# Kernel tuning notes

Hardware: AMD Instinct MI355X
Metric: run time of the kernel (lower is better)

The kernel has to match this reference:

```python
import jax, jax.numpy as jnp
import numpy as np

TEMPERATURE = 0.5
NEG_FILL = -9e15


def setup_inputs() -> dict:
    key = jax.random.key(0)
    k1, k2 = jax.random.split(key)
    B, D = 8192, 128
    z_i = jax.random.normal(k1, (B, D), dtype=jnp.float32)
    z_j = jax.random.normal(k2, (B, D), dtype=jnp.float32)
    return {"z_i": z_i, "z_j": z_j}


def reference(z_i, z_j):
    B = z_i.shape[0]
    N = 2 * B
    z = jnp.concatenate([z_i, z_j], axis=0)              # [2B, D]
    sim = jnp.matmul(z, z.T) / TEMPERATURE               # [2B, 2B]
    # mask out self-similarity on the diagonal
    diag = jnp.eye(N, dtype=bool)
    sim = jnp.where(diag, NEG_FILL, sim)
    # positive pair of row k is row (k+B) mod 2B
    labels = jnp.concatenate([jnp.arange(B, N), jnp.arange(0, B)])
    # CrossEntropyLoss(reduction='sum'): sum_k logsumexp(sim[k]) - sim[k, labels[k]]
    lse = jax.nn.logsumexp(sim, axis=1)                  # [2B]
    pos = sim[jnp.arange(N), labels]                     # [2B]
    loss = jnp.sum(lse - pos)
    return loss / N
```

## Files before the change

kernel.cpp:

```cpp
#include <hip/hip_runtime.h>

#define TEMP    0.5f
#define LOG2E   1.4426950408889634f
#define C2      (LOG2E / TEMP)
#define SQC2    1.6986436f
#define MSHIFT  160.0f
#define LN2     0.6931471805599453f
#define NROWS   16384
#define BHALF   8192
#define DDIM    128
#define PREPB   2048
#define MAINB   512

typedef __bf16 bf16x8 __attribute__((ext_vector_type(8)));
typedef float  f32x16 __attribute__((ext_vector_type(16)));
typedef float  f32x2  __attribute__((ext_vector_type(2)));

__device__ __forceinline__ float fexp2(float x) {
#if __has_builtin(__builtin_amdgcn_exp2f)
  return __builtin_amdgcn_exp2f(x);
#else
  return exp2f(x);
#endif
}

__device__ __forceinline__ unsigned short f2bf(float f) {
  unsigned int u = __float_as_uint(f);
  unsigned int r = (u + 0x7FFFu + ((u >> 16) & 1u)) >> 16;
  return (unsigned short)r;
}


__global__ void k_prep(const float* __restrict__ zi, const float* __restrict__ zj,
                       unsigned short* __restrict__ zbF,
                       float* __restrict__ S, float* __restrict__ Pp,
                       unsigned int* __restrict__ cnt) {
  const int t   = blockIdx.x * 256 + threadIdx.x;
  const int row = t >> 5;
  const int k0  = (t & 31) * 4;
  const float* src = (row < BHALF) ? (zi + (size_t)row * DDIM)
                                   : (zj + (size_t)(row - BHALF) * DDIM);
  float4 v = *reinterpret_cast<const float4*>(src + k0);

  const int g = row >> 5, lo = row & 31, khi = k0 >> 3, j0 = k0 & 7;
  ushort4 o;
  o.x = f2bf(v.x * SQC2); o.y = f2bf(v.y * SQC2);
  o.z = f2bf(v.z * SQC2); o.w = f2bf(v.w * SQC2);
  *reinterpret_cast<ushort4*>(zbF + (size_t)g * 4096 + khi * 256 + lo * 8 + j0) = o;

  float dot = 0.f;
  if (row < BHALF) {
    float4 w = *reinterpret_cast<const float4*>(zj + (size_t)row * DDIM + k0);
    dot = fmaf(v.x, w.x, fmaf(v.y, w.y, fmaf(v.z, w.z, v.w * w.w)));
  }
#pragma unroll
  for (int m = 32; m >= 1; m >>= 1) dot += __shfl_xor(dot, m, 64);
  __shared__ float red[4];
  if ((threadIdx.x & 63) == 0) red[threadIdx.x >> 6] = dot;
  __syncthreads();
  if (threadIdx.x == 0) Pp[blockIdx.x] = red[0] + red[1] + red[2] + red[3];

  if (t < NROWS) S[t] = 0.f;
  if (t == 0) cnt[0] = 0u;
}

template <bool MASK>
__device__ __forceinline__ void expAcc(const f32x16& acc, f32x2& s, int d, int hi) {
#pragma unroll
  for (int k = 0; k < 8; ++k) {
    f32x2 e;
    e.x = fexp2(acc[2 * k]);
    e.y = fexp2(acc[2 * k + 1]);
    if (MASK) {
      const int r0 = 2 * k, r1 = 2 * k + 1;
      if (((r0 & 3) + 8 * (r0 >> 2) + 4 * hi) == d) e.x = 0.f;
      if (((r1 & 3) + 8 * (r1 >> 2) + 4 * hi) == d) e.y = 0.f;
    }
    s += e;
  }
}

#define MFMA_ __builtin_amdgcn_mfma_f32_32x32x16_bf16

__global__ __launch_bounds__(256, 2)
void k_main(const unsigned short* __restrict__ zbF, float* __restrict__ S,
            const float* __restrict__ Pp, unsigned int* __restrict__ cnt,
            float* __restrict__ out) {
  const int wave = threadIdx.x >> 6;
  const int lane = threadIdx.x & 63;
  const int lo = lane & 31;
  const int hi = lane >> 5;
  const int rb = blockIdx.x & 31;
  const int cc = blockIdx.x >> 5;
  const int row0w = rb * 512 + wave * 128;

  bf16x8 b[4][8];
#pragma unroll
  for (int rt = 0; rt < 4; ++rt) {
    const unsigned short* bp = zbF + (size_t)((row0w >> 5) + rt) * 4096 + hi * 256 + lo * 8;
#pragma unroll
    for (int ks = 0; ks < 8; ++ks)
      b[rt][ks] = *reinterpret_cast<const bf16x8*>(bp + ks * 512);
  }

  f32x16 kC;
#pragma unroll
  for (int r = 0; r < 16; ++r) kC[r] = -MSHIFT;

  f32x2 s[4];
#pragma unroll
  for (int rt = 0; rt < 4; ++rt) { s[rt].x = 0.f; s[rt].y = 0.f; }

  const int c0base = cc * 1024;
  const unsigned short* abase = zbF + (size_t)(c0base >> 5) * 4096 + hi * 256 + lo * 8;

  bf16x8 a[8];
#pragma unroll
  for (int ks = 0; ks < 8; ++ks)
    a[ks] = *reinterpret_cast<const bf16x8*>(abase + ks * 512);

  if (((blockIdx.x ^ wave) & 1) != 0) __builtin_amdgcn_s_sleep(4);

  for (int it = 0; it < 32; ++it) {
    const int c0 = c0base + it * 32;
    const int dr = c0 - row0w;
    const bool dg = (unsigned)dr < 128u;
    const int rtd = dg ? (dr >> 5) : -1;

    __builtin_amdgcn_s_setprio(1);
    f32x16 acc0 = MFMA_(a[0], b[0][0], kC, 0, 0, 0);
    f32x16 acc1 = MFMA_(a[0], b[1][0], kC, 0, 0, 0);
#pragma unroll
    for (int ks = 1; ks < 8; ++ks) {
      acc0 = MFMA_(a[ks], b[0][ks], acc0, 0, 0, 0);
      acc1 = MFMA_(a[ks], b[1][ks], acc1, 0, 0, 0);
    }
    __builtin_amdgcn_s_setprio(0);
    if (!dg) {
      expAcc<false>(acc0, s[0], -1, hi);
      expAcc<false>(acc1, s[1], -1, hi);
    } else {
      expAcc<true>(acc0, s[0], rtd == 0 ? lo : -1, hi);
      expAcc<true>(acc1, s[1], rtd == 1 ? lo : -1, hi);
    }

    __builtin_amdgcn_s_setprio(1);
    acc0 = MFMA_(a[0], b[2][0], kC, 0, 0, 0);
    acc1 = MFMA_(a[0], b[3][0], kC, 0, 0, 0);
#pragma unroll
    for (int ks = 1; ks < 8; ++ks) {
      acc0 = MFMA_(a[ks], b[2][ks], acc0, 0, 0, 0);
      acc1 = MFMA_(a[ks], b[3][ks], acc1, 0, 0, 0);
    }
    __builtin_amdgcn_s_setprio(0);

    if (it + 1 < 32) {
      const unsigned short* ap = abase + (size_t)(it + 1) * 4096;
#pragma unroll
      for (int ks = 0; ks < 8; ++ks)
        a[ks] = *reinterpret_cast<const bf16x8*>(ap + ks * 512);
    }

    if (!dg) {
      expAcc<false>(acc0, s[2], -1, hi);
      expAcc<false>(acc1, s[3], -1, hi);
    } else {
      expAcc<true>(acc0, s[2], rtd == 2 ? lo : -1, hi);
      expAcc<true>(acc1, s[3], rtd == 3 ? lo : -1, hi);
    }
  }

#pragma unroll
  for (int rt = 0; rt < 4; ++rt) {
    float v = s[rt].x + s[rt].y;
    v += __shfl_xor(v, 32, 64);
    if (hi == 0) atomicAdd(&S[row0w + rt * 32 + lo], v);
  }

  asm volatile("s_waitcnt vmcnt(0)" ::: "memory");
  __syncthreads();
  __shared__ unsigned int lastFlag;
  if (threadIdx.x == 0) {
    unsigned int old = __hip_atomic_fetch_add(cnt, 1u, __ATOMIC_RELAXED,
                                              __HIP_MEMORY_SCOPE_AGENT);
    lastFlag = (old == (unsigned)(MAINB - 1)) ? 1u : 0u;
  }
  __syncthreads();
  if (lastFlag) {
    __threadfence();
    const int t = threadIdx.x;
    float q = 0.f;
    for (int r = t; r < NROWS; r += 256) {
      float sv = __hip_atomic_load(&S[r], __ATOMIC_RELAXED,
                                   __HIP_MEMORY_SCOPE_AGENT);
      q += LN2 * (MSHIFT + __log2f(sv));
    }
    for (int r = t; r < PREPB; r += 256)
      q -= 4.0f * Pp[r];
    __shared__ float red[256];
    red[t] = q;
    __syncthreads();
    for (int s2 = 128; s2 > 0; s2 >>= 1) {
      if (t < s2) red[t] += red[t + s2];
      __syncthreads();
    }
    if (t == 0) out[0] = red[0] / (float)NROWS;
  }
}

extern "C" void kernel_launch(void* const* d_in, const int* in_sizes, int n_in,
                              void* d_out, int out_size, void* d_ws, size_t ws_size,
                              hipStream_t stream) {
  const float* zi = (const float*)d_in[0];
  const float* zj = (const float*)d_in[1];
  unsigned short* zbF = (unsigned short*)d_ws;
  float* S  = (float*)((char*)d_ws + (size_t)NROWS * DDIM * 2);
  float* Pp = S + NROWS;
  unsigned int* cnt = (unsigned int*)(Pp + PREPB);
  float* out = (float*)d_out;

  hipLaunchKernelGGL(k_prep, dim3(PREPB), dim3(256), 0, stream, zi, zj, zbF, S, Pp, cnt);
  hipLaunchKernelGGL(k_main, dim3(MAINB), dim3(256), 0, stream, zbF, S, Pp, cnt, out);
}
```

Baseline: 144.0 us.

## Fuse prep and main kernels into one persistent kernel with grid barrier

Measured after the change: 210.0 us. 45.8% more time.

```diff
diff --git a/kernel.cpp b/kernel.cpp
--- a/kernel.cpp
+++ b/kernel.cpp
@@ -3,13 +3,12 @@
 #define TEMP    0.5f
 #define LOG2E   1.4426950408889634f
 #define C2      (LOG2E / TEMP)
-#define SQC2    1.6986436f
 #define MSHIFT  160.0f
 #define LN2     0.6931471805599453f
 #define NROWS   16384
 #define BHALF   8192
 #define DDIM    128
-#define PREPB   2048
+#define NCHUNK  2048
 #define MAINB   512
 
 typedef __bf16 bf16x8 __attribute__((ext_vector_type(8)));
@@ -31,46 +30,19 @@
 }
 
 
-__global__ void k_prep(const float* __restrict__ zi, const float* __restrict__ zj,
-                       unsigned short* __restrict__ zbF,
-                       float* __restrict__ S, float* __restrict__ Pp,
-                       unsigned int* __restrict__ cnt) {
-  const int t   = blockIdx.x * 256 + threadIdx.x;
-  const int row = t >> 5;
-  const int k0  = (t & 31) * 4;
-  const float* src = (row < BHALF) ? (zi + (size_t)row * DDIM)
-                                   : (zj + (size_t)(row - BHALF) * DDIM);
-  float4 v = *reinterpret_cast<const float4*>(src + k0);
-
-  const int g = row >> 5, lo = row & 31, khi = k0 >> 3, j0 = k0 & 7;
-  ushort4 o;
-  o.x = f2bf(v.x * SQC2); o.y = f2bf(v.y * SQC2);
-  o.z = f2bf(v.z * SQC2); o.w = f2bf(v.w * SQC2);
-  *reinterpret_cast<ushort4*>(zbF + (size_t)g * 4096 + khi * 256 + lo * 8 + j0) = o;
-
-  float dot = 0.f;
-  if (row < BHALF) {
-    float4 w = *reinterpret_cast<const float4*>(zj + (size_t)row * DDIM + k0);
-    dot = fmaf(v.x, w.x, fmaf(v.y, w.y, fmaf(v.z, w.z, v.w * w.w)));
-  }
-#pragma unroll
-  for (int m = 32; m >= 1; m >>= 1) dot += __shfl_xor(dot, m, 64);
-  __shared__ float red[4];
-  if ((threadIdx.x & 63) == 0) red[threadIdx.x >> 6] = dot;
-  __syncthreads();
-  if (threadIdx.x == 0) Pp[blockIdx.x] = red[0] + red[1] + red[2] + red[3];
-
-  if (t < NROWS) S[t] = 0.f;
-  if (t == 0) cnt[0] = 0u;
-}
-
 template <bool MASK>
 __device__ __forceinline__ void expAcc(const f32x16& acc, f32x2& s, int d, int hi) {
 #pragma unroll
   for (int k = 0; k < 8; ++k) {
+    f32x2 u;
+    u.x = acc[2 * k];
+    u.y = acc[2 * k + 1];
+    const f32x2 c2v = {C2, C2};
+    const f32x2 msv = {-MSHIFT, -MSHIFT};
+    u = __builtin_elementwise_fma(u, c2v, msv);
     f32x2 e;
-    e.x = fexp2(acc[2 * k]);
-    e.y = fexp2(acc[2 * k + 1]);
+    e.x = fexp2(u.x);
+    e.y = fexp2(u.y);
     if (MASK) {
       const int r0 = 2 * k, r1 = 2 * k + 1;
       if (((r0 & 3) + 8 * (r0 >> 2) + 4 * hi) == d) e.x = 0.f;
@@ -83,9 +55,63 @@
 #define MFMA_ __builtin_amdgcn_mfma_f32_32x32x16_bf16
 
 __global__ __launch_bounds__(256, 2)
-void k_main(const unsigned short* __restrict__ zbF, float* __restrict__ S,
-            const float* __restrict__ Pp, unsigned int* __restrict__ cnt,
-            float* __restrict__ out) {
+void k_all(const float* __restrict__ zi, const float* __restrict__ zj,
+           unsigned short* __restrict__ zbF, float* __restrict__ S,
+           float* __restrict__ Pp, unsigned int* __restrict__ cnt,
+           float* __restrict__ out) {
+  __shared__ unsigned int curChunk;
+  __shared__ float red[4];
+
+  unsigned int nmine = 0;
+  for (;;) {
+    if (threadIdx.x == 0)
+      curChunk = __hip_atomic_fetch_add(&cnt[0], 1u, __ATOMIC_RELAXED,
+                                        __HIP_MEMORY_SCOPE_AGENT);
+    __syncthreads();
+    const unsigned int c = curChunk;
+    if (c >= NCHUNK) break;
+
+    const int t   = (int)c * 256 + threadIdx.x;
+    const int row = t >> 5;
+    const int k0  = (t & 31) * 4;
+    const float* src = (row < BHALF) ? (zi + (size_t)row * DDIM)
+                                     : (zj + (size_t)(row - BHALF) * DDIM);
+    float4 v = *reinterpret_cast<const float4*>(src + k0);
+
+    const int g = row >> 5, lo2 = row & 31, khi = k0 >> 3, j0 = k0 & 7;
+    ushort4 o;
+    o.x = f2bf(v.x); o.y = f2bf(v.y); o.z = f2bf(v.z); o.w = f2bf(v.w);
+    *reinterpret_cast<ushort4*>(zbF + (size_t)g * 4096 + khi * 256 + lo2 * 8 + j0) = o;
+
+    float dot = 0.f;
+    if (row < BHALF) {
+      float4 w = *reinterpret_cast<const float4*>(zj + (size_t)row * DDIM + k0);
+      dot = fmaf(v.x, w.x, fmaf(v.y, w.y, fmaf(v.z, w.z, v.w * w.w)));
+    }
+#pragma unroll
+    for (int m = 32; m >= 1; m >>= 1) dot += __shfl_xor(dot, m, 64);
+    if ((threadIdx.x & 63) == 0) red[threadIdx.x >> 6] = dot;
+    __syncthreads();
+    if (threadIdx.x == 0) Pp[c] = red[0] + red[1] + red[2] + red[3];
+    if (t < NROWS) S[t] = 0.f;
+    ++nmine;
+    __syncthreads();
+  }
+
+  __builtin_amdgcn_fence(__ATOMIC_RELEASE, "agent");
+  __syncthreads();
+  if (threadIdx.x == 0 && nmine)
+    __hip_atomic_fetch_add(&cnt[1], nmine, __ATOMIC_RELAXED,
+                           __HIP_MEMORY_SCOPE_AGENT);
+
+  if (threadIdx.x == 0) {
+    while (__hip_atomic_load(&cnt[1], __ATOMIC_RELAXED,
+                             __HIP_MEMORY_SCOPE_AGENT) < NCHUNK)
+      __builtin_amdgcn_s_sleep(16);
+  }
+  __syncthreads();
+  __builtin_amdgcn_fence(__ATOMIC_ACQUIRE, "agent");
+
   const int wave = threadIdx.x >> 6;
   const int lane = threadIdx.x & 63;
   const int lo = lane & 31;
@@ -103,10 +129,7 @@
       b[rt][ks] = *reinterpret_cast<const bf16x8*>(bp + ks * 512);
   }
 
-  f32x16 kC;
-#pragma unroll
-  for (int r = 0; r < 16; ++r) kC[r] = -MSHIFT;
-
+  const f32x16 kZ = {};
   f32x2 s[4];
 #pragma unroll
   for (int rt = 0; rt < 4; ++rt) { s[rt].x = 0.f; s[rt].y = 0.f; }
@@ -128,8 +151,8 @@
     const int rtd = dg ? (dr >> 5) : -1;
 
     __builtin_amdgcn_s_setprio(1);
-    f32x16 acc0 = MFMA_(a[0], b[0][0], kC, 0, 0, 0);
-    f32x16 acc1 = MFMA_(a[0], b[1][0], kC, 0, 0, 0);
+    f32x16 acc0 = MFMA_(a[0], b[0][0], kZ, 0, 0, 0);
+    f32x16 acc1 = MFMA_(a[0], b[1][0], kZ, 0, 0, 0);
 #pragma unroll
     for (int ks = 1; ks < 8; ++ks) {
       acc0 = MFMA_(a[ks], b[0][ks], acc0, 0, 0, 0);
@@ -145,8 +168,8 @@
     }
 
     __builtin_amdgcn_s_setprio(1);
-    acc0 = MFMA_(a[0], b[2][0], kC, 0, 0, 0);
-    acc1 = MFMA_(a[0], b[3][0], kC, 0, 0, 0);
+    acc0 = MFMA_(a[0], b[2][0], kZ, 0, 0, 0);
+    acc1 = MFMA_(a[0], b[3][0], kZ, 0, 0, 0);
 #pragma unroll
     for (int ks = 1; ks < 8; ++ks) {
       acc0 = MFMA_(a[ks], b[2][ks], acc0, 0, 0, 0);
@@ -181,30 +204,34 @@
   __syncthreads();
   __shared__ unsigned int lastFlag;
   if (threadIdx.x == 0) {
-    unsigned int old = __hip_atomic_fetch_add(cnt, 1u, __ATOMIC_RELAXED,
+    unsigned int old = __hip_atomic_fetch_add(&cnt[2], 1u, __ATOMIC_RELAXED,
                                               __HIP_MEMORY_SCOPE_AGENT);
     lastFlag = (old == (unsigned)(MAINB - 1)) ? 1u : 0u;
   }
   __syncthreads();
   if (lastFlag) {
-    __threadfence();
+    __builtin_amdgcn_fence(__ATOMIC_ACQUIRE, "agent");
     const int t = threadIdx.x;
     float q = 0.f;
-    for (int r = t; r < NROWS; r += 256) {
-      float sv = __hip_atomic_load(&S[r], __ATOMIC_RELAXED,
-                                   __HIP_MEMORY_SCOPE_AGENT);
-      q += LN2 * (MSHIFT + __log2f(sv));
-    }
-    for (int r = t; r < PREPB; r += 256)
-      q -= 4.0f * Pp[r];
-    __shared__ float red[256];
-    red[t] = q;
+    const float4* S4 = reinterpret_cast<const float4*>(S);
+    for (int i = t; i < NROWS / 4; i += 256) {
+      float4 sv = S4[i];
+      q += LN2 * (4.0f * MSHIFT + __log2f(sv.x) + __log2f(sv.y) +
+                  __log2f(sv.z) + __log2f(sv.w));
+    }
+    const float4* P4 = reinterpret_cast<const float4*>(Pp);
+    for (int i = t; i < NCHUNK / 4; i += 256) {
+      float4 p = P4[i];
+      q -= 4.0f * (p.x + p.y + p.z + p.w);
+    }
+    __shared__ float redf[256];
+    redf[t] = q;
     __syncthreads();
     for (int s2 = 128; s2 > 0; s2 >>= 1) {
-      if (t < s2) red[t] += red[t + s2];
+      if (t < s2) redf[t] += redf[t + s2];
       __syncthreads();
     }
-    if (t == 0) out[0] = red[0] / (float)NROWS;
+    if (t == 0) out[0] = redf[0] / (float)NROWS;
   }
 }
 
@@ -216,9 +243,10 @@
   unsigned short* zbF = (unsigned short*)d_ws;
   float* S  = (float*)((char*)d_ws + (size_t)NROWS * DDIM * 2);
   float* Pp = S + NROWS;
-  unsigned int* cnt = (unsigned int*)(Pp + PREPB);
+  unsigned int* cnt = (unsigned int*)(Pp + NCHUNK);
   float* out = (float*)d_out;
 
-  hipLaunchKernelGGL(k_prep, dim3(PREPB), dim3(256), 0, stream, zi, zj, zbF, S, Pp, cnt);
-  hipLaunchKernelGGL(k_main, dim3(MAINB), dim3(256), 0, stream, zbF, S, Pp, cnt, out);
-}
+  hipMemsetAsync(cnt, 0, 3 * sizeof(unsigned int), stream);
+  hipLaunchKernelGGL(k_all, dim3(MAINB), dim3(256), 0, stream,
+                     zi, zj, zbF, S, Pp, cnt, out);
+}
```
